# Performance work log

Hardware: AMD Instinct MI355X
Metric: run time of the kernel (lower is better)

The kernel has to match this reference:

```python
import jax, jax.numpy as jnp
import numpy as np

MARGIN = 1.0
EPS = 1e-8  # torch.cosine_similarity default eps


def _cosine(a, b):
    num = jnp.sum(a * b, axis=1)
    den = jnp.maximum(jnp.linalg.norm(a, axis=1) * jnp.linalg.norm(b, axis=1), EPS)
    return num / den


def setup_inputs() -> dict:
    key = jax.random.key(0)
    k1, k2 = jax.random.split(key)
    B, D = 8192, 512
    anchor = jax.random.normal(k1, (B, D), dtype=jnp.float32)
    positive = jax.random.normal(k2, (B, D), dtype=jnp.float32)
    return {"anchor": anchor, "positive": positive}


def reference(anchor, positive):
    B = positive.shape[0]
    a_n = anchor / jnp.linalg.norm(anchor, axis=1, keepdims=True)
    p_n = positive / jnp.linalg.norm(positive, axis=1, keepdims=True)
    sim = a_n @ p_n.T                      # [B, B] cosine similarity
    mask = 1.0 - jnp.eye(B, dtype=sim.dtype)
    sim = sim * mask                       # zero diagonal
    # margin branch of NegariveSampler (margin=1): abs(sim - margin), zeros -> -inf, argmax
    score = jnp.abs(sim - MARGIN) * mask
    score = jnp.where(score == 0.0, -jnp.inf, score)
    neg_idx = jnp.argmax(score, axis=1)    # [B]
    neg = p_n[neg_idx]                     # gather normalized positives as negatives
    cos_ap = _cosine(anchor, positive)
    cos_an = _cosine(anchor, neg)
    loss = jax.nn.relu(MARGIN + cos_ap - cos_an)
    return loss.mean()
```

## Files before the change

### kernel.cpp

```cpp
#include <hip/hip_runtime.h>
#include <stdint.h>

typedef int   i32x8 __attribute__((ext_vector_type(8)));
typedef float f32x4 __attribute__((ext_vector_type(4)));

#define B_ROWS 8192
#define D_DIM  512

__global__ __launch_bounds__(256) void norm_kernel(
    const float* __restrict__ anchor, const float* __restrict__ positive,
    uint32_t* __restrict__ a8, uint32_t* __restrict__ p8,
    float* __restrict__ cos_ap)
{
  const int wave = threadIdx.x >> 6, lane = threadIdx.x & 63;
  const int r = blockIdx.x * 4 + wave;

  const float4* av = (const float4*)(anchor   + (size_t)r * D_DIM) + lane * 2;
  const float4* pv = (const float4*)(positive + (size_t)r * D_DIM) + lane * 2;
  float4 a0 = av[0], a1 = av[1];
  float4 p0 = pv[0], p1 = pv[1];

  float sa = a0.x*a0.x + a0.y*a0.y + a0.z*a0.z + a0.w*a0.w
           + a1.x*a1.x + a1.y*a1.y + a1.z*a1.z + a1.w*a1.w;
  float sp = p0.x*p0.x + p0.y*p0.y + p0.z*p0.z + p0.w*p0.w
           + p1.x*p1.x + p1.y*p1.y + p1.z*p1.z + p1.w*p1.w;
  float dp = a0.x*p0.x + a0.y*p0.y + a0.z*p0.z + a0.w*p0.w
           + a1.x*p1.x + a1.y*p1.y + a1.z*p1.z + a1.w*p1.w;

#pragma unroll
  for (int d = 1; d < 64; d <<= 1) {
    sa += __shfl_xor(sa, d);
    sp += __shfl_xor(sp, d);
    dp += __shfl_xor(dp, d);
  }

  const float na = sqrtf(sa), np = sqrtf(sp);
  const float ia = 1.0f / na, ip = 1.0f / np;

  float na0 = a0.x*ia, na1 = a0.y*ia, na2 = a0.z*ia, na3 = a0.w*ia;
  float na4 = a1.x*ia, na5 = a1.y*ia, na6 = a1.z*ia, na7 = a1.w*ia;
  float np0 = p0.x*ip, np1 = p0.y*ip, np2 = p0.z*ip, np3 = p0.w*ip;
  float np4 = p1.x*ip, np5 = p1.y*ip, np6 = p1.z*ip, np7 = p1.w*ip;

  uint32_t aw0 = __builtin_amdgcn_cvt_pk_fp8_f32(na0, na1, 0,  false);
  aw0          = __builtin_amdgcn_cvt_pk_fp8_f32(na2, na3, aw0, true);
  uint32_t aw1 = __builtin_amdgcn_cvt_pk_fp8_f32(na4, na5, 0,  false);
  aw1          = __builtin_amdgcn_cvt_pk_fp8_f32(na6, na7, aw1, true);
  uint32_t pw0 = __builtin_amdgcn_cvt_pk_fp8_f32(np0, np1, 0,  false);
  pw0          = __builtin_amdgcn_cvt_pk_fp8_f32(np2, np3, pw0, true);
  uint32_t pw1 = __builtin_amdgcn_cvt_pk_fp8_f32(np4, np5, 0,  false);
  pw1          = __builtin_amdgcn_cvt_pk_fp8_f32(np6, np7, pw1, true);

  ((uint2*)a8)[(size_t)r * 64 + lane] = make_uint2(aw0, aw1);
  ((uint2*)p8)[(size_t)r * 64 + lane] = make_uint2(pw0, pw1);

  if (lane == 0) cos_ap[r] = dp / fmaxf(na * np, 1e-8f);
}

__device__ __forceinline__ void load16_to_lds(const void* g, void* l) {
  __builtin_amdgcn_global_load_lds(
      (__attribute__((address_space(1))) uint32_t*)(uintptr_t)(g),
      (__attribute__((address_space(3))) uint32_t*)(uintptr_t)(l),
      16, 0, 0);
}

__global__ __launch_bounds__(256) void simmin_kernel(
    const uint8_t* __restrict__ a8, const uint8_t* __restrict__ p8,
    float* __restrict__ partial)
{
  __shared__ __attribute__((aligned(16))) uint8_t Alds[128 * 128];
  __shared__ __attribute__((aligned(16))) uint8_t Plds[128 * 128];
  __shared__ float redmin[256];

  const int tid  = threadIdx.x;
  const int lane = tid & 63;
  const int wave = tid >> 6;
  const int waveM = wave >> 1, waveN = wave & 1;
  const int quad = lane >> 4;
  const int l15  = lane & 15;
  const int blockRow = blockIdx.x, blockCol = blockIdx.y;

  f32x4 acc[4][4];
  const f32x4 zero = {0.f, 0.f, 0.f, 0.f};
#pragma unroll
  for (int i = 0; i < 4; i++)
#pragma unroll
    for (int j = 0; j < 4; j++) acc[i][j] = zero;

  const int srow = lane >> 3;
  const int sk   = (lane & 7) ^ srow;
  const uint8_t* aBase = a8 + (size_t)(blockRow * 128) * D_DIM;
  const uint8_t* pBase = p8 + (size_t)(blockCol * 128) * D_DIM;

  for (int k0 = 0; k0 < D_DIM; k0 += 128) {
#pragma unroll
    for (int c = 0; c < 4; c++) {
      const int chunk = wave * 4 + c;
      const size_t goff = (size_t)(chunk * 8 + srow) * D_DIM + k0 + sk * 16;
      load16_to_lds(aBase + goff, &Alds[chunk * 1024]);
      load16_to_lds(pBase + goff, &Plds[chunk * 1024]);
    }
    __syncthreads();

    i32x8 af[4], bfr[4];
#pragma unroll
    for (int mf = 0; mf < 4; mf++) {
      const int r = waveM * 64 + mf * 16 + l15;
      const int rx = r & 7;
      const int4 lo = *(const int4*)&Alds[r * 128 + (((quad * 2 + 0) ^ rx) * 16)];
      const int4 hi = *(const int4*)&Alds[r * 128 + (((quad * 2 + 1) ^ rx) * 16)];
      af[mf] = (i32x8){lo.x, lo.y, lo.z, lo.w, hi.x, hi.y, hi.z, hi.w};
    }
#pragma unroll
    for (int nf = 0; nf < 4; nf++) {
      const int r = waveN * 64 + nf * 16 + l15;
      const int rx = r & 7;
      const int4 lo = *(const int4*)&Plds[r * 128 + (((quad * 2 + 0) ^ rx) * 16)];
      const int4 hi = *(const int4*)&Plds[r * 128 + (((quad * 2 + 1) ^ rx) * 16)];
      bfr[nf] = (i32x8){lo.x, lo.y, lo.z, lo.w, hi.x, hi.y, hi.z, hi.w};
    }

#pragma unroll
    for (int mf = 0; mf < 4; mf++)
#pragma unroll
      for (int nf = 0; nf < 4; nf++)
        acc[mf][nf] = __builtin_amdgcn_mfma_scale_f32_16x16x128_f8f6f4(
            af[mf], bfr[nf], acc[mf][nf],
            0, 0,
            0, 0x7F7F7F7F,
            0, 0x7F7F7F7F);

    __syncthreads();
  }

  const int rowTileBase = blockRow * 128 + waveM * 64;
  const int colTileBase = blockCol * 128 + waveN * 64;

  float rm[4][4];
#pragma unroll
  for (int mf = 0; mf < 4; mf++)
#pragma unroll
    for (int r = 0; r < 4; r++) rm[mf][r] = 3.0e38f;

#pragma unroll
  for (int mf = 0; mf < 4; mf++) {
#pragma unroll
    for (int nf = 0; nf < 4; nf++) {
      const int col = colTileBase + nf * 16 + l15;
#pragma unroll
      for (int r = 0; r < 4; r++) {
        const int row = rowTileBase + mf * 16 + quad * 4 + r;
        const float v = acc[mf][nf][r];
        rm[mf][r] = (row == col) ? rm[mf][r] : fminf(rm[mf][r], v);
      }
    }
  }
#pragma unroll
  for (int d = 1; d < 16; d <<= 1)
#pragma unroll
    for (int mf = 0; mf < 4; mf++)
#pragma unroll
      for (int r = 0; r < 4; r++)
        rm[mf][r] = fminf(rm[mf][r], __shfl_xor(rm[mf][r], d));

  if (l15 == 0) {
#pragma unroll
    for (int mf = 0; mf < 4; mf++)
#pragma unroll
      for (int r = 0; r < 4; r++)
        redmin[waveN * 128 + waveM * 64 + mf * 16 + quad * 4 + r] = rm[mf][r];
  }
  __syncthreads();

  if (tid < 128) {
    const float m = fminf(redmin[tid], redmin[128 + tid]);
    partial[(size_t)blockCol * B_ROWS + blockRow * 128 + tid] = m;
  }
}

__global__ __launch_bounds__(256) void finalize_kernel(
    const float* __restrict__ partial, const float* __restrict__ cos_ap,
    float* __restrict__ out)
{
  const int r = blockIdx.x * 256 + threadIdx.x;
  float m = 3.0e38f;
#pragma unroll 8
  for (int c = 0; c < 64; c++) m = fminf(m, partial[(size_t)c * B_ROWS + r]);
  float loss = fmaxf(0.0f, 1.0f + cos_ap[r] - m);

  for (int off = 32; off > 0; off >>= 1) loss += __shfl_down(loss, off);
  __shared__ float s[4];
  const int wave = threadIdx.x >> 6, lane = threadIdx.x & 63;
  if (lane == 0) s[wave] = loss;
  __syncthreads();
  if (threadIdx.x == 0) {
    const float t = (s[0] + s[1] + s[2] + s[3]) * (1.0f / (float)B_ROWS);
    atomicAdd(out, t);
  }
}

extern "C" void kernel_launch(void* const* d_in, const int* in_sizes, int n_in,
                              void* d_out, int out_size, void* d_ws, size_t ws_size,
                              hipStream_t stream) {
  const float* anchor   = (const float*)d_in[0];
  const float* positive = (const float*)d_in[1];

  char* ws = (char*)d_ws;
  uint32_t* a8     = (uint32_t*)(ws);
  uint32_t* p8     = (uint32_t*)(ws + (4ull << 20));
  float*    cos_ap = (float*)(ws + (8ull << 20));
  float*    partial = (float*)(ws + (8ull << 20) + (64ull << 10));
  float*    out = (float*)d_out;

  hipMemsetAsync(out, 0, sizeof(float), stream);
  norm_kernel<<<B_ROWS / 4, 256, 0, stream>>>(anchor, positive, a8, p8, cos_ap);
  simmin_kernel<<<dim3(64, 64), 256, 0, stream>>>((const uint8_t*)a8,
                                                  (const uint8_t*)p8, partial);
  finalize_kernel<<<32, 256, 0, stream>>>(partial, cos_ap, out);
}
```

Measured before the change: 141.9 us.

## Double-buffer LDS staging and replace partial-min buffer with atomic min

The similarity kernel now double-buffers its A/P tiles in LDS, prefetching the next K slice while MFMAs run on the current one, and drops the trailing barrier. Per-block row minima are merged with an atomicMin on an order-preserving uint encoding instead of being written to a 64x8192 partial array, so finalize becomes a single block with no memset. The aim is to hide global-load latency and cut partial-buffer traffic, at the cost of doubled LDS (lower occupancy hint of 2) and atomic contention.

```diff
diff --git a/kernel.cpp b/kernel.cpp
--- a/kernel.cpp
+++ b/kernel.cpp
@@ -6,11 +6,20 @@
 
 #define B_ROWS 8192
 #define D_DIM  512
+
+__device__ __forceinline__ uint32_t enc_f32(float f) {
+  uint32_t s = __float_as_uint(f);
+  return (s & 0x80000000u) ? ~s : (s | 0x80000000u);
+}
+__device__ __forceinline__ float dec_f32(uint32_t e) {
+  uint32_t s = (e & 0x80000000u) ? (e ^ 0x80000000u) : ~e;
+  return __uint_as_float(s);
+}
 
 __global__ __launch_bounds__(256) void norm_kernel(
     const float* __restrict__ anchor, const float* __restrict__ positive,
     uint32_t* __restrict__ a8, uint32_t* __restrict__ p8,
-    float* __restrict__ cos_ap)
+    float* __restrict__ cos_ap, uint32_t* __restrict__ minenc)
 {
   const int wave = threadIdx.x >> 6, lane = threadIdx.x & 63;
   const int r = blockIdx.x * 4 + wave;
@@ -54,7 +63,10 @@
   ((uint2*)a8)[(size_t)r * 64 + lane] = make_uint2(aw0, aw1);
   ((uint2*)p8)[(size_t)r * 64 + lane] = make_uint2(pw0, pw1);
 
-  if (lane == 0) cos_ap[r] = dp / fmaxf(na * np, 1e-8f);
+  if (lane == 0) {
+    cos_ap[r] = dp / fmaxf(na * np, 1e-8f);
+    minenc[r] = 0xFFFFFFFFu;
+  }
 }
 
 __device__ __forceinline__ void load16_to_lds(const void* g, void* l) {
@@ -64,12 +76,12 @@
       16, 0, 0);
 }
 
-__global__ __launch_bounds__(256) void simmin_kernel(
+__global__ __launch_bounds__(256, 2) void simmin_kernel(
     const uint8_t* __restrict__ a8, const uint8_t* __restrict__ p8,
-    float* __restrict__ partial)
+    uint32_t* __restrict__ minenc)
 {
-  __shared__ __attribute__((aligned(16))) uint8_t Alds[128 * 128];
-  __shared__ __attribute__((aligned(16))) uint8_t Plds[128 * 128];
+  __shared__ __attribute__((aligned(16))) uint8_t Alds[2][128 * 128];
+  __shared__ __attribute__((aligned(16))) uint8_t Plds[2][128 * 128];
   __shared__ float redmin[256];
 
   const int tid  = threadIdx.x;
@@ -92,33 +104,42 @@
   const uint8_t* aBase = a8 + (size_t)(blockRow * 128) * D_DIM;
   const uint8_t* pBase = p8 + (size_t)(blockCol * 128) * D_DIM;
 
-  for (int k0 = 0; k0 < D_DIM; k0 += 128) {
+  auto stage = [&](int k0, int buf) {
 #pragma unroll
     for (int c = 0; c < 4; c++) {
       const int chunk = wave * 4 + c;
       const size_t goff = (size_t)(chunk * 8 + srow) * D_DIM + k0 + sk * 16;
-      load16_to_lds(aBase + goff, &Alds[chunk * 1024]);
-      load16_to_lds(pBase + goff, &Plds[chunk * 1024]);
-    }
+      load16_to_lds(aBase + goff, &Alds[buf][chunk * 1024]);
+      load16_to_lds(pBase + goff, &Plds[buf][chunk * 1024]);
+    }
+  };
+
+  stage(0, 0);
+
+#pragma unroll
+  for (int k = 0; k < 4; k++) {
     __syncthreads();
+    const int buf = k & 1;
 
     i32x8 af[4], bfr[4];
 #pragma unroll
     for (int mf = 0; mf < 4; mf++) {
       const int r = waveM * 64 + mf * 16 + l15;
       const int rx = r & 7;
-      const int4 lo = *(const int4*)&Alds[r * 128 + (((quad * 2 + 0) ^ rx) * 16)];
-      const int4 hi = *(const int4*)&Alds[r * 128 + (((quad * 2 + 1) ^ rx) * 16)];
+      const int4 lo = *(const int4*)&Alds[buf][r * 128 + (((quad * 2 + 0) ^ rx) * 16)];
+      const int4 hi = *(const int4*)&Alds[buf][r * 128 + (((quad * 2 + 1) ^ rx) * 16)];
       af[mf] = (i32x8){lo.x, lo.y, lo.z, lo.w, hi.x, hi.y, hi.z, hi.w};
     }
 #pragma unroll
     for (int nf = 0; nf < 4; nf++) {
       const int r = waveN * 64 + nf * 16 + l15;
       const int rx = r & 7;
-      const int4 lo = *(const int4*)&Plds[r * 128 + (((quad * 2 + 0) ^ rx) * 16)];
-      const int4 hi = *(const int4*)&Plds[r * 128 + (((quad * 2 + 1) ^ rx) * 16)];
+      const int4 lo = *(const int4*)&Plds[buf][r * 128 + (((quad * 2 + 0) ^ rx) * 16)];
+      const int4 hi = *(const int4*)&Plds[buf][r * 128 + (((quad * 2 + 1) ^ rx) * 16)];
       bfr[nf] = (i32x8){lo.x, lo.y, lo.z, lo.w, hi.x, hi.y, hi.z, hi.w};
     }
+
+    if (k < 3) stage((k + 1) * 128, (k + 1) & 1);
 
 #pragma unroll
     for (int mf = 0; mf < 4; mf++)
@@ -129,8 +150,6 @@
             0, 0,
             0, 0x7F7F7F7F,
             0, 0x7F7F7F7F);
-
-    __syncthreads();
   }
 
   const int rowTileBase = blockRow * 128 + waveM * 64;
@@ -174,29 +193,26 @@
 
   if (tid < 128) {
     const float m = fminf(redmin[tid], redmin[128 + tid]);
-    partial[(size_t)blockCol * B_ROWS + blockRow * 128 + tid] = m;
+    atomicMin(&minenc[blockRow * 128 + tid], enc_f32(m));
   }
 }
 
 __global__ __launch_bounds__(256) void finalize_kernel(
-    const float* __restrict__ partial, const float* __restrict__ cos_ap,
+    const uint32_t* __restrict__ minenc, const float* __restrict__ cos_ap,
     float* __restrict__ out)
 {
-  const int r = blockIdx.x * 256 + threadIdx.x;
-  float m = 3.0e38f;
+  float sum = 0.0f;
 #pragma unroll 8
-  for (int c = 0; c < 64; c++) m = fminf(m, partial[(size_t)c * B_ROWS + r]);
-  float loss = fmaxf(0.0f, 1.0f + cos_ap[r] - m);
-
-  for (int off = 32; off > 0; off >>= 1) loss += __shfl_down(loss, off);
+  for (int r = threadIdx.x; r < B_ROWS; r += 256)
+    sum += fmaxf(0.0f, 1.0f + cos_ap[r] - dec_f32(minenc[r]));
+
+#pragma unroll
+  for (int d = 1; d < 64; d <<= 1) sum += __shfl_xor(sum, d);
   __shared__ float s[4];
-  const int wave = threadIdx.x >> 6, lane = threadIdx.x & 63;
-  if (lane == 0) s[wave] = loss;
+  if ((threadIdx.x & 63) == 0) s[threadIdx.x >> 6] = sum;
   __syncthreads();
-  if (threadIdx.x == 0) {
-    const float t = (s[0] + s[1] + s[2] + s[3]) * (1.0f / (float)B_ROWS);
-    atomicAdd(out, t);
-  }
+  if (threadIdx.x == 0)
+    out[0] = (s[0] + s[1] + s[2] + s[3]) * (1.0f / (float)B_ROWS);
 }
 
 extern "C" void kernel_launch(void* const* d_in, const int* in_sizes, int n_in,
@@ -209,12 +225,12 @@
   uint32_t* a8     = (uint32_t*)(ws);
   uint32_t* p8     = (uint32_t*)(ws + (4ull << 20));
   float*    cos_ap = (float*)(ws + (8ull << 20));
-  float*    partial = (float*)(ws + (8ull << 20) + (64ull << 10));
+  uint32_t* minenc = (uint32_t*)(ws + (8ull << 20) + (32ull << 10));
   float*    out = (float*)d_out;
 
-  hipMemsetAsync(out, 0, sizeof(float), stream);
-  norm_kernel<<<B_ROWS / 4, 256, 0, stream>>>(anchor, positive, a8, p8, cos_ap);
+  norm_kernel<<<B_ROWS / 4, 256, 0, stream>>>(anchor, positive, a8, p8,
+                                              cos_ap, minenc);
   simmin_kernel<<<dim3(64, 64), 256, 0, stream>>>((const uint8_t*)a8,
-                                                  (const uint8_t*)p8, partial);
-  finalize_kernel<<<32, 256, 0, stream>>>(partial, cos_ap, out);
-}
+                                                  (const uint8_t*)p8, minenc);
+  finalize_kernel<<<1, 256, 0, stream>>>(minenc, cos_ap, out);
+}
```

Measured after the change: 124.6 us. 12.2% less time.

## Fuse finalize into simmin via atomic min and last-block reduction

Applied to the files above, without the earlier changes.

Removes the memset and the separate finalize kernel. The similarity kernel now does an atomicMin on order-preserving encoded floats into per-row minima, and the last block to finish (found through an atomic counter) computes the loss mean. It also remaps the 1D grid so consecutive blocks share P tiles for better L2 reuse, interleaves B-fragment loads with the MFMAs to cut register pressure, and sets launch bounds to 3 blocks per CU. The cost is 128 atomics per block plus a serial tail reduction done by a single block.

```diff
diff --git a/kernel.cpp b/kernel.cpp
--- a/kernel.cpp
+++ b/kernel.cpp
@@ -6,11 +6,22 @@
 
 #define B_ROWS 8192
 #define D_DIM  512
+#define GRID_SIMMIN 4096
+
+__device__ __forceinline__ uint32_t enc_f32(float f) {
+  uint32_t s = __float_as_uint(f);
+  return (s & 0x80000000u) ? ~s : (s | 0x80000000u);
+}
+__device__ __forceinline__ float dec_f32(uint32_t e) {
+  uint32_t s = (e & 0x80000000u) ? (e ^ 0x80000000u) : ~e;
+  return __uint_as_float(s);
+}
 
 __global__ __launch_bounds__(256) void norm_kernel(
     const float* __restrict__ anchor, const float* __restrict__ positive,
     uint32_t* __restrict__ a8, uint32_t* __restrict__ p8,
-    float* __restrict__ cos_ap)
+    float* __restrict__ cos_ap, uint32_t* __restrict__ minenc,
+    uint32_t* __restrict__ donecnt)
 {
   const int wave = threadIdx.x >> 6, lane = threadIdx.x & 63;
   const int r = blockIdx.x * 4 + wave;
@@ -54,7 +65,11 @@
   ((uint2*)a8)[(size_t)r * 64 + lane] = make_uint2(aw0, aw1);
   ((uint2*)p8)[(size_t)r * 64 + lane] = make_uint2(pw0, pw1);
 
-  if (lane == 0) cos_ap[r] = dp / fmaxf(na * np, 1e-8f);
+  if (lane == 0) {
+    cos_ap[r] = dp / fmaxf(na * np, 1e-8f);
+    minenc[r] = 0xFFFFFFFFu;
+  }
+  if (blockIdx.x == 0 && threadIdx.x == 0) *donecnt = 0u;
 }
 
 __device__ __forceinline__ void load16_to_lds(const void* g, void* l) {
@@ -64,13 +79,15 @@
       16, 0, 0);
 }
 
-__global__ __launch_bounds__(256) void simmin_kernel(
+__global__ __launch_bounds__(256, 3) void simmin_kernel(
     const uint8_t* __restrict__ a8, const uint8_t* __restrict__ p8,
-    float* __restrict__ partial)
+    uint32_t* __restrict__ minenc, const float* __restrict__ cos_ap,
+    uint32_t* __restrict__ donecnt, float* __restrict__ out)
 {
   __shared__ __attribute__((aligned(16))) uint8_t Alds[128 * 128];
   __shared__ __attribute__((aligned(16))) uint8_t Plds[128 * 128];
   __shared__ float redmin[256];
+  __shared__ int   isLast;
 
   const int tid  = threadIdx.x;
   const int lane = tid & 63;
@@ -78,7 +95,10 @@
   const int waveM = wave >> 1, waveN = wave & 1;
   const int quad = lane >> 4;
   const int l15  = lane & 15;
-  const int blockRow = blockIdx.x, blockCol = blockIdx.y;
+
+  const int bid = blockIdx.x;
+  const int blockRow = (bid & 7) * 8 + ((bid >> 3) & 7);
+  const int blockCol = bid >> 6;
 
   f32x4 acc[4][4];
   const f32x4 zero = {0.f, 0.f, 0.f, 0.f};
@@ -102,7 +122,7 @@
     }
     __syncthreads();
 
-    i32x8 af[4], bfr[4];
+    i32x8 af[4];
 #pragma unroll
     for (int mf = 0; mf < 4; mf++) {
       const int r = waveM * 64 + mf * 16 + l15;
@@ -117,19 +137,15 @@
       const int rx = r & 7;
       const int4 lo = *(const int4*)&Plds[r * 128 + (((quad * 2 + 0) ^ rx) * 16)];
       const int4 hi = *(const int4*)&Plds[r * 128 + (((quad * 2 + 1) ^ rx) * 16)];
-      bfr[nf] = (i32x8){lo.x, lo.y, lo.z, lo.w, hi.x, hi.y, hi.z, hi.w};
-    }
-
-#pragma unroll
-    for (int mf = 0; mf < 4; mf++)
-#pragma unroll
-      for (int nf = 0; nf < 4; nf++)
+      const i32x8 bfr = (i32x8){lo.x, lo.y, lo.z, lo.w, hi.x, hi.y, hi.z, hi.w};
+#pragma unroll
+      for (int mf = 0; mf < 4; mf++)
         acc[mf][nf] = __builtin_amdgcn_mfma_scale_f32_16x16x128_f8f6f4(
-            af[mf], bfr[nf], acc[mf][nf],
+            af[mf], bfr, acc[mf][nf],
             0, 0,
             0, 0x7F7F7F7F,
             0, 0x7F7F7F7F);
-
+    }
     __syncthreads();
   }
 
@@ -174,28 +190,28 @@
 
   if (tid < 128) {
     const float m = fminf(redmin[tid], redmin[128 + tid]);
-    partial[(size_t)blockCol * B_ROWS + blockRow * 128 + tid] = m;
-  }
-}
-
-__global__ __launch_bounds__(256) void finalize_kernel(
-    const float* __restrict__ partial, const float* __restrict__ cos_ap,
-    float* __restrict__ out)
-{
-  const int r = blockIdx.x * 256 + threadIdx.x;
-  float m = 3.0e38f;
-#pragma unroll 8
-  for (int c = 0; c < 64; c++) m = fminf(m, partial[(size_t)c * B_ROWS + r]);
-  float loss = fmaxf(0.0f, 1.0f + cos_ap[r] - m);
-
-  for (int off = 32; off > 0; off >>= 1) loss += __shfl_down(loss, off);
-  __shared__ float s[4];
-  const int wave = threadIdx.x >> 6, lane = threadIdx.x & 63;
-  if (lane == 0) s[wave] = loss;
+    atomicMin(&minenc[blockRow * 128 + tid], enc_f32(m));
+  }
+
+  __threadfence();
+  if (tid == 0) {
+    const uint32_t old = atomicAdd(donecnt, 1u);
+    isLast = (old == (uint32_t)(GRID_SIMMIN - 1));
+  }
   __syncthreads();
-  if (threadIdx.x == 0) {
-    const float t = (s[0] + s[1] + s[2] + s[3]) * (1.0f / (float)B_ROWS);
-    atomicAdd(out, t);
+  if (isLast) {
+    float sum = 0.0f;
+    for (int r = tid; r < B_ROWS; r += 256) {
+      const uint32_t e = atomicOr(&minenc[r], 0u);
+      sum += fmaxf(0.0f, 1.0f + cos_ap[r] - dec_f32(e));
+    }
+#pragma unroll
+    for (int d = 1; d < 64; d <<= 1) sum += __shfl_xor(sum, d);
+    if ((tid & 63) == 0) redmin[tid >> 6] = sum;
+    __syncthreads();
+    if (tid == 0)
+      out[0] = (redmin[0] + redmin[1] + redmin[2] + redmin[3])
+               * (1.0f / (float)B_ROWS);
   }
 }
 
@@ -206,15 +222,16 @@
   const float* positive = (const float*)d_in[1];
 
   char* ws = (char*)d_ws;
-  uint32_t* a8     = (uint32_t*)(ws);
-  uint32_t* p8     = (uint32_t*)(ws + (4ull << 20));
-  float*    cos_ap = (float*)(ws + (8ull << 20));
-  float*    partial = (float*)(ws + (8ull << 20) + (64ull << 10));
+  uint32_t* a8      = (uint32_t*)(ws);
+  uint32_t* p8      = (uint32_t*)(ws + (4ull << 20));
+  float*    cos_ap  = (float*)(ws + (8ull << 20));
+  uint32_t* minenc  = (uint32_t*)(ws + (8ull << 20) + (32ull << 10));
+  uint32_t* donecnt = (uint32_t*)(ws + (8ull << 20) + (64ull << 10));
   float*    out = (float*)d_out;
 
-  hipMemsetAsync(out, 0, sizeof(float), stream);
-  norm_kernel<<<B_ROWS / 4, 256, 0, stream>>>(anchor, positive, a8, p8, cos_ap);
-  simmin_kernel<<<dim3(64, 64), 256, 0, stream>>>((const uint8_t*)a8,
-                                                  (const uint8_t*)p8, partial);
-  finalize_kernel<<<32, 256, 0, stream>>>(partial, cos_ap, out);
-}
+  norm_kernel<<<B_ROWS / 4, 256, 0, stream>>>(anchor, positive, a8, p8,
+                                              cos_ap, minenc, donecnt);
+  simmin_kernel<<<GRID_SIMMIN, 256, 0, stream>>>((const uint8_t*)a8,
+                                                 (const uint8_t*)p8, minenc,
+                                                 cos_ap, donecnt, out);
+}
```

Result: slower. 347.4 us (+144.8%).
